# Kernel optimization log

Hardware: AMD Instinct MI355X
Metric: run time of the kernel (lower is better)

## Reference

```python
import jax, jax.numpy as jnp
import numpy as np

EPS = 1e-6

def _conv1x1(x, w, bias):
    # x: [b,cin,h,w], w: [cout,cin]
    y = jnp.einsum('bchw,oc->bohw', x, w)
    return y + bias[None, :, None, None]

def _maxpool2(x):
    b, c, h, w = x.shape
    return x.reshape(b, c, h // 2, 2, w // 2, 2).max(axis=(3, 5))

def _up2_align_corners(x):
    # bilinear upsample x2, align_corners=True (matches torch nn.Upsample)
    b, c, h, w = x.shape
    oh, ow = 2 * h, 2 * w
    ys = jnp.linspace(0.0, h - 1.0, oh)
    xs = jnp.linspace(0.0, w - 1.0, ow)
    y0 = jnp.floor(ys).astype(jnp.int32); y1 = jnp.minimum(y0 + 1, h - 1)
    x0 = jnp.floor(xs).astype(jnp.int32); x1 = jnp.minimum(x0 + 1, w - 1)
    ty = (ys - y0).reshape(1, 1, oh, 1)
    tx = (xs - x0).reshape(1, 1, 1, ow)
    r0 = x[:, :, y0, :]; r1 = x[:, :, y1, :]           # [b,c,oh,w]
    v00 = r0[:, :, :, x0]; v01 = r0[:, :, :, x1]       # [b,c,oh,ow]
    v10 = r1[:, :, :, x0]; v11 = r1[:, :, :, x1]
    return (1 - ty) * ((1 - tx) * v00 + tx * v01) + ty * ((1 - tx) * v10 + tx * v11)

def _norm_corr(fm):
    # fm: [b,N,N], indexed [b,p,q]; ReLU then L2-normalize over q for each p
    m = jnp.maximum(fm, 0.0)
    norm = jnp.sqrt(jnp.sum(m * m, axis=2, keepdims=True) + EPS)
    return m / norm

def setup_inputs() -> dict:
    key = jax.random.key(0)
    ks = jax.random.split(key, 8)
    d = {
        'xa': jax.random.normal(ks[0], (8, 256, 64, 64), jnp.float32),
        'xb': jax.random.normal(ks[1], (8, 256, 64, 64), jnp.float32),
        'conv_w': jax.random.normal(ks[2], (1024, 256), jnp.float32) * 0.02,
        'conv_b': jax.random.normal(ks[3], (1024,), jnp.float32) * 0.02,
        'We': jax.random.normal(ks[4], (1024, 1024), jnp.float32) * 0.02,
        'We2': jax.random.normal(ks[5], (1024, 1024), jnp.float32) * 0.02,
        'conv2_w': jax.random.normal(ks[6], (256, 1024), jnp.float32) * 0.02,
        'conv2_b': jax.random.normal(ks[7], (256,), jnp.float32) * 0.02,
    }
    return d

def reference(xa, xb, conv_w, conv_b, We, We2, conv2_w, conv2_b):
    fa = _maxpool2(_conv1x1(xa, conv_w, conv_b))   # [b,c,h,w]
    fb = _maxpool2(_conv1x1(xb, conv_w, conv_b))
    b, c, h, w = fa.shape
    N = h * w
    Fa = fa.reshape(b, c, N)                        # [b,c,N]
    Fb = fb.reshape(b, c, N)
    Fb_t = jnp.swapaxes(Fb, 1, 2)                   # [b,N,c]
    Fa_t = jnp.swapaxes(Fa, 1, 2)
    # fm[b,p,q] = (linear_e(Fb_t) @ Fa)
    fm = jnp.einsum('bpc,cd,bdq->bpq', Fb_t, We.T, Fa)
    Mab = _norm_corr(fm)                            # normalized over q per p
    fm2 = jnp.einsum('bpc,cd,bdq->bpq', Fa_t, We2.T, Fb)
    Mba = _norm_corr(fm2)
    # torch: bmm(corr.view(b,N,N), feat) with corr_flat[b,q,p] = Mn[b,p,q]
    en_a = jnp.einsum('bpq,bpk->bqk', Mab, Fa_t)    # [b,N,c]
    en_b = jnp.einsum('bpq,bpk->bqk', Mba, Fb_t)
    # faithful reinterpretation (torch .view(b,c,h,w) on a [b,N,c] tensor)
    en_a = en_a.reshape(b, c, h, w)
    en_b = en_b.reshape(b, c, h, w)
    en_a = _conv1x1(_up2_align_corners(en_a), conv2_w, conv2_b)
    en_b = _conv1x1(_up2_align_corners(en_b), conv2_w, conv2_b)
    return (en_a, en_b)
```

## Files before the change

### kernel.cpp

```cpp
#include <hip/hip_runtime.h>

typedef unsigned short u16;
typedef short bfrag __attribute__((ext_vector_type(8)));
typedef float facc  __attribute__((ext_vector_type(4)));

__device__ __forceinline__ float bf2f(u16 u) {
    union { unsigned int i; float f; } v; v.i = ((unsigned int)u) << 16; return v.f;
}
__device__ __forceinline__ u16 f2bf(float f) {
    union { float f; unsigned int i; } v; v.f = f;
    unsigned int r = v.i + 0x7FFFu + ((v.i >> 16) & 1u);
    return (u16)(r >> 16);
}

__device__ __forceinline__ void store_out(u16* p, float v)   { *p = f2bf(v); }
__device__ __forceinline__ void store_out(float* p, float v) { *p = v; }

__device__ __forceinline__ void gl2lds16(const u16* g, char* l) {
    __builtin_amdgcn_global_load_lds(
        (const __attribute__((address_space(1))) unsigned int*)g,
        (__attribute__((address_space(3))) unsigned int*)l,
        16, 0, 0);
}

__global__ void cvt4_k(const float* __restrict__ s0, u16* __restrict__ d0,
                       const float* __restrict__ s1, u16* __restrict__ d1,
                       const float* __restrict__ s2, u16* __restrict__ d2,
                       const float* __restrict__ s3, u16* __restrict__ d3) {
    int i = blockIdx.x * blockDim.x + threadIdx.x;
    if (i < 262144)        d0[i] = f2bf(s0[i]);
    else if (i < 1310720)  d1[i - 262144] = f2bf(s1[i - 262144]);
    else if (i < 2359296)  d2[i - 1310720] = f2bf(s2[i - 1310720]);
    else                   d3[i - 2359296] = f2bf(s3[i - 2359296]);
}

__global__ void transpose_in_k(const float* __restrict__ srcA,
                               const float* __restrict__ srcB,
                               u16* __restrict__ dst) {
    __shared__ u16 tile[64][65];
    const long SX = 1048576;
    const int z  = blockIdx.z;
    const int c0 = blockIdx.x * 64;
    const int r0 = blockIdx.y * 64;
    const int x  = threadIdx.x;
    const int y0 = threadIdx.y;
    const float* s = (z < 8 ? srcA : srcB) + (size_t)(z & 7) * SX;
    for (int i = 0; i < 8; ++i) {
        int r = y0 + i * 8;
        tile[r][x] = f2bf(s[(size_t)(r0 + r) * 4096 + c0 + x]);
    }
    __syncthreads();
    u16* d = dst + (size_t)z * SX;
    for (int i = 0; i < 8; ++i) {
        int c = y0 + i * 8;
        d[(size_t)(c0 + c) * 256 + r0 + x] = tile[x][c];
    }
}

template <typename OutT, int MODE, bool PAIRED>
__global__ __launch_bounds__(256)
void gemm_nt(const u16* __restrict__ A0, const u16* __restrict__ A1, long strideA,
             const u16* __restrict__ B0, const u16* __restrict__ B1, long strideBT,
             OutT* __restrict__ C, long strideC, u16* __restrict__ CT,
             const float* __restrict__ bias, int M, int N, int K) {
    constexpr bool POOL = (MODE == 2);
    __shared__ __align__(16) char smem[32768];
    char* As = smem;
    char* Bs = smem + 16384;

    const int gx = gridDim.x, gy = gridDim.y;
    long id = blockIdx.x + (long)gx * (blockIdx.y + (long)gy * blockIdx.z);
    long total = (long)gx * gy * gridDim.z;
    long nid = (id & 7) * (total >> 3) + (id >> 3);
    const int bx = (int)(nid % gx);
    long rr = nid / gx;
    const int by = (int)(rr % gy);
    const int b  = (int)(rr / gy);

    const int m0 = bx * 128;
    const int n0 = by * 128;

    const u16* Ab; const u16* Bb;
    if (PAIRED) {
        const int bl = b & 7;
        Ab = (b < 8 ? A0 : A1) + (size_t)bl * strideA;
        Bb = (b < 8 ? B0 : B1) + (size_t)bl * strideBT;
    } else {
        Ab = A0 + (size_t)b * strideA;
        Bb = B0 + (size_t)b * strideBT;
    }

    const int t    = threadIdx.x;
    const int lane = t & 63;
    const int w    = t >> 6;
    const int wm   = (w & 1) * 64;
    const int wn   = (w >> 1) * 64;
    const int q    = lane >> 4;
    const int ln   = lane & 15;

    const int s0 = w * 64 + lane;
    const int s1 = s0 + 256;
    const int r0s = s0 >> 2, c0s = (s0 & 3) * 8;
    const int r1s = s1 >> 2, c1s = (s1 & 3) * 8;

    const int gr0 = POOL ? ((2 * by + ((r0s >> 1) & 1)) * 64 + (r0s >> 2) * 2 + (r0s & 1))
                         : (n0 + r0s);
    const int gr1 = POOL ? ((2 * by + ((r1s >> 1) & 1)) * 64 + (r1s >> 2) * 2 + (r1s & 1))
                         : (n0 + r1s);

    const u16* pA0 = Ab + (size_t)(m0 + r0s) * K + c0s;
    const u16* pA1 = Ab + (size_t)(m0 + r1s) * K + c1s;
    const u16* pB0 = Bb + (size_t)gr0 * K + c0s;
    const u16* pB1 = Bb + (size_t)gr1 * K + c1s;

    facc acc[4][4];
    for (int i = 0; i < 4; ++i)
        for (int j = 0; j < 4; ++j)
            acc[i][j] = (facc)0.0f;

    const int nK = K >> 6;
    for (int kt = 0; kt < nK; ++kt) {
        const int k0 = kt << 6;
        gl2lds16(pA0 + k0,      As + s0 * 16);
        gl2lds16(pA1 + k0,      As + s1 * 16);
        gl2lds16(pA0 + k0 + 32, As + 8192 + s0 * 16);
        gl2lds16(pA1 + k0 + 32, As + 8192 + s1 * 16);
        gl2lds16(pB0 + k0,      Bs + s0 * 16);
        gl2lds16(pB1 + k0,      Bs + s1 * 16);
        gl2lds16(pB0 + k0 + 32, Bs + 8192 + s0 * 16);
        gl2lds16(pB1 + k0 + 32, Bs + 8192 + s1 * 16);
        __syncthreads();
        for (int j = 0; j < 2; ++j) {
            const char* Aj = As + j * 8192;
            const char* Bj = Bs + j * 8192;
            bfrag af[4], bfr[4];
            for (int mt = 0; mt < 4; ++mt)
                af[mt] = *reinterpret_cast<const bfrag*>(Aj + (wm + mt * 16 + ln) * 64 + q * 16);
            for (int nt = 0; nt < 4; ++nt)
                bfr[nt] = *reinterpret_cast<const bfrag*>(Bj + (wn + nt * 16 + ln) * 64 + q * 16);
            for (int mt = 0; mt < 4; ++mt)
                for (int nt = 0; nt < 4; ++nt)
                    acc[mt][nt] = __builtin_amdgcn_mfma_f32_16x16x32_bf16(af[mt], bfr[nt], acc[mt][nt], 0, 0, 0);
        }
        __syncthreads();
    }

    if (POOL) {
        u16* Cp  = (u16*)C + (size_t)b * strideC;
        u16* CTb = CT + (size_t)b * strideC;
        const int a = ln >> 2;
        for (int mt = 0; mt < 4; ++mt) {
            const int chb = wm + mt * 16 + q * 4;
            float bs0 = bias[m0 + chb + 0];
            float bs1 = bias[m0 + chb + 1];
            float bs2 = bias[m0 + chb + 2];
            float bs3 = bias[m0 + chb + 3];
            for (int nt = 0; nt < 4; ++nt) {
                const int xp = (wn >> 2) + nt * 4 + a;
                float p0 = acc[mt][nt][0] + bs0;
                float p1 = acc[mt][nt][1] + bs1;
                float p2 = acc[mt][nt][2] + bs2;
                float p3 = acc[mt][nt][3] + bs3;
                p0 = fmaxf(p0, __shfl_xor(p0, 1, 64)); p0 = fmaxf(p0, __shfl_xor(p0, 2, 64));
                p1 = fmaxf(p1, __shfl_xor(p1, 1, 64)); p1 = fmaxf(p1, __shfl_xor(p1, 2, 64));
                p2 = fmaxf(p2, __shfl_xor(p2, 1, 64)); p2 = fmaxf(p2, __shfl_xor(p2, 2, 64));
                p3 = fmaxf(p3, __shfl_xor(p3, 1, 64)); p3 = fmaxf(p3, __shfl_xor(p3, 2, 64));
                float s01 = (ln & 1) ? p1 : p0;
                float s23 = (ln & 1) ? p3 : p2;
                float sel = (ln & 2) ? s23 : s01;
                Cp[(size_t)(m0 + chb + (ln & 3)) * 1024 + by * 32 + xp] = f2bf(sel);
                if ((ln & 3) == 0) {
                    uint2 pk;
                    pk.x = (unsigned)f2bf(p0) | ((unsigned)f2bf(p1) << 16);
                    pk.y = (unsigned)f2bf(p2) | ((unsigned)f2bf(p3) << 16);
                    *reinterpret_cast<uint2*>(&CTb[(size_t)(by * 32 + xp) * 1024 + m0 + chb]) = pk;
                }
            }
        }
    } else if (MODE == 0) {
        u16* Cb = (u16*)C + (size_t)b * strideC;
        u16* dump = (u16*)smem;
        for (int mt = 0; mt < 4; ++mt)
            for (int nt = 0; nt < 4; ++nt)
                for (int r = 0; r < 4; ++r)
                    dump[(wm + mt * 16 + q * 4 + r) * 128 + wn + nt * 16 + ln] = f2bf(acc[mt][nt][r]);
        __syncthreads();
        for (int i = 0; i < 8; ++i) {
            const int row = w * 32 + i * 4 + (lane >> 4);
            const uint4 v = *reinterpret_cast<const uint4*>(dump + row * 128 + (lane & 15) * 8);
            *reinterpret_cast<uint4*>(Cb + (size_t)(m0 + row) * N + n0 + (lane & 15) * 8) = v;
        }
    } else {
        OutT* Cb = C + (size_t)b * strideC;
        for (int mt = 0; mt < 4; ++mt) {
            const int rbase = m0 + wm + mt * 16 + q * 4;
            for (int nt = 0; nt < 4; ++nt) {
                const int col = n0 + wn + nt * 16 + ln;
                for (int r = 0; r < 4; ++r)
                    store_out(&Cb[(size_t)(rbase + r) * N + col], acc[mt][nt][r] + bias[rbase + r]);
            }
        }
    }
}

__global__ void norm_rk(const u16* __restrict__ fm, float* __restrict__ rinv) {
    __shared__ float red[4];
    const long row = blockIdx.x;
    const u16* p = fm + row * 1024;
    const int t = threadIdx.x;
    uint2 raw = *reinterpret_cast<const uint2*>(p + t * 4);
    float v0 = fmaxf(bf2f((u16)(raw.x & 0xFFFF)), 0.f);
    float v1 = fmaxf(bf2f((u16)(raw.x >> 16)), 0.f);
    float v2 = fmaxf(bf2f((u16)(raw.y & 0xFFFF)), 0.f);
    float v3 = fmaxf(bf2f((u16)(raw.y >> 16)), 0.f);
    float s = v0 * v0 + v1 * v1 + v2 * v2 + v3 * v3;
    for (int off = 32; off; off >>= 1) s += __shfl_down(s, off, 64);
    if ((t & 63) == 0) red[t >> 6] = s;
    __syncthreads();
    if (t == 0)
        rinv[row] = 1.0f / sqrtf(red[0] + red[1] + red[2] + red[3] + 1e-6f);
}

__global__ void transpose_scale_k(const u16* __restrict__ src,
                                  const float* __restrict__ rinv,
                                  u16* __restrict__ dst) {
    __shared__ u16 tile[64][65];
    const long S = 1048576;
    const int b  = blockIdx.z;
    const int c0 = blockIdx.x * 64;
    const int r0 = blockIdx.y * 64;
    const int x  = threadIdx.x;
    const int y0 = threadIdx.y;
    const u16* s = src + (size_t)b * S;
    const float* rv = rinv + (size_t)b * 1024;
    for (int i = 0; i < 8; ++i) {
        int r = y0 + i * 8;
        float v = fmaxf(bf2f(s[(size_t)(r0 + r) * 1024 + c0 + x]), 0.f) * rv[r0 + r];
        tile[r][x] = f2bf(v);
    }
    __syncthreads();
    u16* d = dst + (size_t)b * S;
    for (int i = 0; i < 8; ++i) {
        int c = y0 + i * 8;
        d[(size_t)(c0 + c) * 1024 + r0 + x] = tile[x][c];
    }
}

__global__ void upsample_k(const float* __restrict__ V, float* __restrict__ out, int total) {
    int idx = blockIdx.x * blockDim.x + threadIdx.x;
    if (idx >= total) return;
    int X  = idx & 63;
    int Y  = (idx >> 6) & 63;
    long bo = idx >> 12;
    const float* p = V + bo * 1024;
    const float sc = 31.0f / 63.0f;
    float ys = Y * sc;
    float xs = X * sc;
    int y0 = (int)ys; int x0 = (int)xs;
    int y1 = y0 + 1; if (y1 > 31) y1 = 31;
    int x1 = x0 + 1; if (x1 > 31) x1 = 31;
    float ty = ys - y0, tx = xs - x0;
    float v00 = p[y0 * 32 + x0], v01 = p[y0 * 32 + x1];
    float v10 = p[y1 * 32 + x0], v11 = p[y1 * 32 + x1];
    out[idx] = (1.f - ty) * ((1.f - tx) * v00 + tx * v01) + ty * ((1.f - tx) * v10 + tx * v11);
}

extern "C" void kernel_launch(void* const* d_in, const int* in_sizes, int n_in,
                              void* d_out, int out_size, void* d_ws, size_t ws_size,
                              hipStream_t stream) {
    const float* xa      = (const float*)d_in[0];
    const float* xb      = (const float*)d_in[1];
    const float* conv_w  = (const float*)d_in[2];
    const float* conv_b  = (const float*)d_in[3];
    const float* We      = (const float*)d_in[4];
    const float* We2     = (const float*)d_in[5];
    const float* conv2_w = (const float*)d_in[6];
    const float* conv2_b = (const float*)d_in[7];
    float* out = (float*)d_out;
    char* ws = (char*)d_ws;

    const long S1M = 1048576;
    const long MiB = 1048576;

    u16*   XT  = (u16*)(ws + 0);
    u16*   T1  = (u16*)(ws + 0);
    u16*   MT  = (u16*)(ws + 0);
    u16*   FA  = (u16*)(ws + 32 * MiB);
    u16*   FB  = (u16*)(ws + 48 * MiB);
    u16*   FAT = (u16*)(ws + 64 * MiB);
    u16*   FBT = (u16*)(ws + 80 * MiB);
    float* V   = (float*)(ws + 64 * MiB);
    u16*   FM  = (u16*)(ws + 96 * MiB);
    u16*   Z   = (u16*)(ws + 96 * MiB);
    u16*   CW  = (u16*)(ws + 128 * MiB);
    u16*   WE  = (u16*)(ws + 128 * MiB + 524288);
    u16*   WE2 = (u16*)(ws + 128 * MiB + 2621440);
    u16*   C2W = (u16*)(ws + 128 * MiB + 4718592);
    float* RIV = (float*)(ws + 128 * MiB + 5242880);

    const dim3 tb64(64, 8);

    cvt4_k<<<10240, 256, 0, stream>>>(conv_w, CW, We, WE, We2, WE2, conv2_w, C2W);

    transpose_in_k<<<dim3(64, 4, 16), tb64, 0, stream>>>(xa, xb, XT);

    gemm_nt<u16, 2, false><<<dim3(8, 32, 16), 256, 0, stream>>>(
        CW, CW, 0, XT, XT, S1M, FA, S1M, FAT, conv_b, 1024, 4096, 256);

    gemm_nt<u16, 0, true><<<dim3(8, 8, 16), 256, 0, stream>>>(
        FBT, FAT, S1M, WE, WE2, 0, T1, S1M, nullptr, nullptr, 1024, 1024, 1024);

    gemm_nt<u16, 0, true><<<dim3(8, 8, 16), 256, 0, stream>>>(
        T1, T1 + 8 * S1M, S1M, FAT, FBT, S1M, FM, S1M, nullptr, nullptr, 1024, 1024, 1024);

    norm_rk<<<16384, 256, 0, stream>>>(FM, RIV);

    transpose_scale_k<<<dim3(16, 16, 16), tb64, 0, stream>>>(FM, RIV, MT);

    gemm_nt<u16, 0, true><<<dim3(8, 8, 16), 256, 0, stream>>>(
        FA, FB, S1M, MT, MT + 8 * S1M, S1M, Z, S1M, nullptr, nullptr, 1024, 1024, 1024);

    gemm_nt<float, 1, false><<<dim3(2, 8, 16), 256, 0, stream>>>(
        C2W, C2W, 0, Z, Z, S1M, V, 256L * 1024, nullptr, conv2_b, 256, 1024, 1024);

    upsample_k<<<65536, 256, 0, stream>>>(V, out, 16 * 256 * 4096);
}
```

Measured before the change: 424.0 us.

## Add 256x256-tile 8-wave pipelined GEMM kernel for the three 1024^3 batched GEMMs

Adds a new bf16 GEMM kernel that uses 256x256 output tiles with 8 waves, double-buffered LDS filled by direct global-to-LDS loads with an XOR swizzle, and interleaved load/MFMA phases separated by barriers and s_setprio. It also remaps block IDs across groups of eight for better L2 locality. The three square 1024x1024x1024 batched GEMMs are switched to this kernel. The aim is more data reuse per tile and overlap of memory traffic with matrix math, at the cost of 128KB LDS per block, one block per CU, and only 256 blocks per launch.

```diff
diff --git a/kernel.cpp b/kernel.cpp
--- a/kernel.cpp
+++ b/kernel.cpp
@@ -203,6 +203,158 @@
     }
 }
 
+#define BAR8() do { asm volatile("" ::: "memory"); __builtin_amdgcn_s_barrier(); asm volatile("" ::: "memory"); } while (0)
+#define VM6() asm volatile("s_waitcnt vmcnt(6)" ::: "memory")
+#define VM0() asm volatile("s_waitcnt vmcnt(0)" ::: "memory")
+
+#define LDA8(BUF, MH) \
+    _Pragma("unroll") for (int mf = 0; mf < 4; ++mf) { \
+        _Pragma("unroll") for (int ks = 0; ks < 2; ++ks) \
+            a[mf][ks] = *reinterpret_cast<const bfrag*>(Ab8 + (BUF) * 32768 + \
+                (wr * 128 + ((MH) * 4 + mf) * 16 + ln) * 128 + (((ks * 4 + q) ^ ln7) << 4)); }
+
+#define LDB8(BUF, NH) \
+    _Pragma("unroll") for (int nf = 0; nf < 2; ++nf) { \
+        _Pragma("unroll") for (int ks = 0; ks < 2; ++ks) \
+            bb[(NH) * 2 + nf][ks] = *reinterpret_cast<const bfrag*>(Bb8 + (BUF) * 32768 + \
+                (wc * 64 + ((NH) * 2 + nf) * 16 + ln) * 128 + (((ks * 4 + q) ^ ln7) << 4)); }
+
+#define MM8(MH, NH) \
+    _Pragma("unroll") for (int mf = 0; mf < 4; ++mf) \
+    _Pragma("unroll") for (int nf = 0; nf < 2; ++nf) \
+    _Pragma("unroll") for (int ks = 0; ks < 2; ++ks) \
+        acc[(MH) * 4 + mf][(NH) * 2 + nf] = __builtin_amdgcn_mfma_f32_16x16x32_bf16( \
+            a[mf][ks], bb[(NH) * 2 + nf][ks], acc[(MH) * 4 + mf][(NH) * 2 + nf], 0, 0, 0);
+
+#define STA8(KT, BUF, H, R) gl2lds16(pAs + (size_t)((H) * 128 + (R) * 8) * K + (KT) * 64, \
+        Ab8 + (BUF) * 32768 + (H) * 16384 + (w * 2 + (R)) * 1024 + lane * 16)
+#define STB8(KT, BUF, H, R) gl2lds16(pBs + (size_t)((H) * 128 + (R) * 8) * K + (KT) * 64, \
+        Bb8 + (BUF) * 32768 + (H) * 16384 + (w * 2 + (R)) * 1024 + lane * 16)
+
+template <bool PAIRED>
+__global__ __launch_bounds__(512, 1)
+void gemm8_nt(const u16* __restrict__ A0, const u16* __restrict__ A1, long strideA,
+              const u16* __restrict__ B0, const u16* __restrict__ B1, long strideBT,
+              u16* __restrict__ C, long strideC, int N, int K) {
+    __shared__ __align__(16) char smem8[131072];
+    char* Ab8 = smem8;
+    char* Bb8 = smem8 + 65536;
+
+    const int gx = gridDim.x, gy = gridDim.y;
+    long id = blockIdx.x + (long)gx * (blockIdx.y + (long)gy * blockIdx.z);
+    long total = (long)gx * gy * gridDim.z;
+    long nid = (id & 7) * (total >> 3) + (id >> 3);
+    const int bx = (int)(nid % gx);
+    long rr = nid / gx;
+    const int by = (int)(rr % gy);
+    const int b  = (int)(rr / gy);
+    const int m0 = bx * 256, n0 = by * 256;
+
+    const u16* Ab; const u16* Bb;
+    if (PAIRED) {
+        const int bl = b & 7;
+        Ab = (b < 8 ? A0 : A1) + (size_t)bl * strideA;
+        Bb = (b < 8 ? B0 : B1) + (size_t)bl * strideBT;
+    } else {
+        Ab = A0 + (size_t)b * strideA;
+        Bb = B0 + (size_t)b * strideBT;
+    }
+
+    const int t    = threadIdx.x;
+    const int lane = t & 63;
+    const int w    = t >> 6;
+    const int wr   = w >> 2;
+    const int wc   = w & 3;
+    const int q    = lane >> 4;
+    const int ln   = lane & 15;
+    const int ln7  = ln & 7;
+    const int l8   = lane >> 3;
+    const int l7   = lane & 7;
+
+    const u16* pAs = Ab + (size_t)(m0 + w * 16 + l8) * K + (l7 ^ l8) * 8;
+    const u16* pBs = Bb + (size_t)(n0 + w * 16 + l8) * K + (l7 ^ l8) * 8;
+
+    facc acc[8][4];
+    #pragma unroll
+    for (int i = 0; i < 8; ++i)
+        #pragma unroll
+        for (int j = 0; j < 4; ++j)
+            acc[i][j] = (facc)0.0f;
+
+    bfrag a[4][2];
+    bfrag bb[4][2];
+
+    const int nIter = K >> 7;
+
+    STB8(0, 0, 0, 0); STB8(0, 0, 0, 1); STB8(0, 0, 1, 0); STB8(0, 0, 1, 1);
+    STA8(0, 0, 0, 0); STA8(0, 0, 0, 1); STA8(0, 0, 1, 0); STA8(0, 0, 1, 1);
+    STB8(1, 1, 0, 0); STB8(1, 1, 0, 1); STB8(1, 1, 1, 0); STB8(1, 1, 1, 1);
+    STA8(1, 1, 0, 0); STA8(1, 1, 0, 1);
+    VM6();
+    BAR8();
+
+    for (int i = 0; i < nIter; ++i) {
+        const bool more = (i + 1 < nIter);
+        const int t1 = 2 * i + 1, t2 = 2 * i + 2, t3 = 2 * i + 3;
+
+        LDA8(0, 0); LDB8(0, 0);
+        STA8(t1, 1, 1, 0); STA8(t1, 1, 1, 1);
+        BAR8();
+        __builtin_amdgcn_s_setprio(1); MM8(0, 0); __builtin_amdgcn_s_setprio(0);
+        BAR8();
+        LDB8(0, 1);
+        BAR8();
+        __builtin_amdgcn_s_setprio(1); MM8(0, 1); __builtin_amdgcn_s_setprio(0);
+        BAR8();
+        LDA8(0, 1);
+        if (more) { STB8(t2, 0, 0, 0); STB8(t2, 0, 0, 1); STB8(t2, 0, 1, 0); STB8(t2, 0, 1, 1); }
+        BAR8();
+        __builtin_amdgcn_s_setprio(1); MM8(1, 0); __builtin_amdgcn_s_setprio(0);
+        BAR8();
+        if (more) { STA8(t2, 0, 0, 0); STA8(t2, 0, 0, 1); VM6(); } else { VM0(); }
+        BAR8();
+        __builtin_amdgcn_s_setprio(1); MM8(1, 1); __builtin_amdgcn_s_setprio(0);
+        BAR8();
+        LDA8(1, 0); LDB8(1, 0);
+        if (more) { STA8(t2, 0, 1, 0); STA8(t2, 0, 1, 1); }
+        BAR8();
+        __builtin_amdgcn_s_setprio(1); MM8(0, 0); __builtin_amdgcn_s_setprio(0);
+        BAR8();
+        LDB8(1, 1);
+        BAR8();
+        __builtin_amdgcn_s_setprio(1); MM8(0, 1); __builtin_amdgcn_s_setprio(0);
+        BAR8();
+        LDA8(1, 1);
+        if (more) { STB8(t3, 1, 0, 0); STB8(t3, 1, 0, 1); STB8(t3, 1, 1, 0); STB8(t3, 1, 1, 1); }
+        BAR8();
+        __builtin_amdgcn_s_setprio(1); MM8(1, 0); __builtin_amdgcn_s_setprio(0);
+        BAR8();
+        if (more) { STA8(t3, 1, 0, 0); STA8(t3, 1, 0, 1); VM6(); } else { VM0(); }
+        BAR8();
+        __builtin_amdgcn_s_setprio(1); MM8(1, 1); __builtin_amdgcn_s_setprio(0);
+        BAR8();
+    }
+
+    u16* dump = (u16*)smem8;
+    #pragma unroll
+    for (int mf = 0; mf < 8; ++mf)
+        #pragma unroll
+        for (int nf = 0; nf < 4; ++nf)
+            #pragma unroll
+            for (int r = 0; r < 4; ++r)
+                dump[(wr * 128 + mf * 16 + q * 4 + r) * 256 + wc * 64 + nf * 16 + ln] =
+                    f2bf(acc[mf][nf][r]);
+    BAR8();
+    u16* Cb = C + (size_t)b * strideC;
+    #pragma unroll
+    for (int it = 0; it < 16; ++it) {
+        int linear = t + it * 512;
+        int row = linear >> 5, c16 = linear & 31;
+        uint4 v = *reinterpret_cast<const uint4*>(dump + row * 256 + c16 * 8);
+        *reinterpret_cast<uint4*>(Cb + (size_t)(m0 + row) * N + n0 + c16 * 8) = v;
+    }
+}
+
 __global__ void norm_rk(const u16* __restrict__ fm, float* __restrict__ rinv) {
     __shared__ float red[4];
     const long row = blockIdx.x;
@@ -307,18 +459,18 @@
     gemm_nt<u16, 2, false><<<dim3(8, 32, 16), 256, 0, stream>>>(
         CW, CW, 0, XT, XT, S1M, FA, S1M, FAT, conv_b, 1024, 4096, 256);
 
-    gemm_nt<u16, 0, true><<<dim3(8, 8, 16), 256, 0, stream>>>(
-        FBT, FAT, S1M, WE, WE2, 0, T1, S1M, nullptr, nullptr, 1024, 1024, 1024);
-
-    gemm_nt<u16, 0, true><<<dim3(8, 8, 16), 256, 0, stream>>>(
-        T1, T1 + 8 * S1M, S1M, FAT, FBT, S1M, FM, S1M, nullptr, nullptr, 1024, 1024, 1024);
+    gemm8_nt<true><<<dim3(4, 4, 16), 512, 0, stream>>>(
+        FBT, FAT, S1M, WE, WE2, 0, T1, S1M, 1024, 1024);
+
+    gemm8_nt<true><<<dim3(4, 4, 16), 512, 0, stream>>>(
+        T1, T1 + 8 * S1M, S1M, FAT, FBT, S1M, FM, S1M, 1024, 1024);
 
     norm_rk<<<16384, 256, 0, stream>>>(FM, RIV);
 
     transpose_scale_k<<<dim3(16, 16, 16), tb64, 0, stream>>>(FM, RIV, MT);
 
-    gemm_nt<u16, 0, true><<<dim3(8, 8, 16), 256, 0, stream>>>(
-        FA, FB, S1M, MT, MT + 8 * S1M, S1M, Z, S1M, nullptr, nullptr, 1024, 1024, 1024);
+    gemm8_nt<true><<<dim3(4, 4, 16), 512, 0, stream>>>(
+        FA, FB, S1M, MT, MT + 8 * S1M, S1M, Z, S1M, 1024, 1024);
 
     gemm_nt<float, 1, false><<<dim3(2, 8, 16), 256, 0, stream>>>(
         C2W, C2W, 0, Z, Z, S1M, V, 256L * 1024, nullptr, conv2_b, 256, 1024, 1024);
```

After: 387.2 us. 1.1x faster.
